# Optimization experiments

Hardware: AMD Instinct MI355X
Metric: run time of the kernel (lower is better)

Reference implementation:

```python
import jax, jax.numpy as jnp
import numpy as np

EPS = 1e-7

def segment_softmax(logits, seg, num_segments):
    # Numerically-stable softmax over edges grouped by destination node,
    # applied independently per feature column (logits: [E, D]).
    m = jax.ops.segment_max(logits, seg, num_segments=num_segments)  # [N, D]
    e = jnp.exp(logits - m[seg])                                     # [E, D]
    s = jax.ops.segment_sum(e, seg, num_segments=num_segments)       # [N, D]
    return e / s[seg]

def setup_inputs() -> dict:
    key = jax.random.key(0)
    N, E, D_IN, D_OUT = 50000, 800000, 64, 64
    ks = jax.random.split(key, 4)
    x = jax.random.normal(ks[0], (N, D_IN), dtype=jnp.float32)
    edge_index = jax.random.randint(ks[1], (2, E), 0, N, dtype=jnp.int64)
    # nn.Linear(in_feat, out_feat) params
    W = jax.random.normal(ks[2], (D_OUT, D_IN), dtype=jnp.float32) * (1.0 / np.sqrt(D_IN))
    b = jax.random.normal(ks[3], (D_OUT,), dtype=jnp.float32) * 0.01
    beta = jnp.ones((1,), dtype=jnp.float32)  # aggr='softmax_sg' beta parameter
    return {"x": x, "W": W, "b": b, "beta": beta, "edge_index": edge_index}

def reference(x, W, b, beta, edge_index):
    N = x.shape[0]
    dst = edge_index[0]  # scatter / softmax segment ids
    src = edge_index[1]  # gather ids
    # gather + ReLU + eps
    edge_msg = jax.nn.relu(x[src]) + EPS                    # [E, D]
    # softmax_sg aggregation: softmax of beta*msg over incoming edges of each dst
    a = segment_softmax(beta * edge_msg, dst, N)            # [E, D]
    h = jax.ops.segment_sum(edge_msg * a, dst, num_segments=N)  # [N, D]
    # final Linear
    return h @ W.T + b
```

## Files before the change

### kernel.cpp

```cpp
#include <hip/hip_runtime.h>
#include <hip/hip_fp16.h>

#define EPS 1e-7f
#define EPB 4096
#define CSTRIDE 16
#define SUBB 4
#define GS 65

__device__ __forceinline__ void pack_body(const float4* __restrict__ x4,
                                          short4* __restrict__ xh, int i, int nq) {
    if (i < nq) {
        float4 v = x4[i];
        short4 o;
        o.x = __half_as_short(__float2half_rn(fmaxf(v.x, 0.f) + EPS));
        o.y = __half_as_short(__float2half_rn(fmaxf(v.y, 0.f) + EPS));
        o.z = __half_as_short(__float2half_rn(fmaxf(v.z, 0.f) + EPS));
        o.w = __half_as_short(__float2half_rn(fmaxf(v.w, 0.f) + EPS));
        xh[i] = o;
    }
}

__global__ __launch_bounds__(256) void part_kernel(const float4* __restrict__ x4,
                                                   short4* __restrict__ xh, int nq,
                                                   int packBlocks,
                                                   const int* __restrict__ ei, int E,
                                                   int CAPB,
                                                   int* __restrict__ cursor,
                                                   unsigned int* __restrict__ partArr) {
    int bb = blockIdx.x;
    int tid = threadIdx.x;
    if (bb < packBlocks) {
        pack_body(x4, xh, bb * 256 + tid, nq);
        return;
    }
    __shared__ int hist[256];
    __shared__ int off[256];
    int blk = bb - packBlocks;
    hist[tid] = 0;
    __syncthreads();

    int base = blk * EPB;
    int dd[16], ss[16], bk[16], rk[16];
    #pragma unroll
    for (int k = 0; k < 16; ++k) {
        int e = base + k * 256 + tid;
        bk[k] = -1;
        if (e < E) {
            dd[k] = ei[e];
            ss[k] = ei[E + e];
            bk[k] = dd[k] >> 8;
            rk[k] = atomicAdd(&hist[bk[k]], 1);
        }
    }
    __syncthreads();
    int hv = hist[tid];
    if (hv > 0) off[tid] = atomicAdd(&cursor[tid * CSTRIDE], hv);
    __syncthreads();
    #pragma unroll
    for (int k = 0; k < 16; ++k) {
        if (bk[k] >= 0) {
            int idx = off[bk[k]] + rk[k];
            if (idx < CAPB)
                partArr[(size_t)bk[k] * CAPB + idx] =
                    ((unsigned int)dd[k] << 16) | (unsigned int)(ss[k] & 0xFFFF);
        }
    }
}

__global__ __launch_bounds__(256) void build_kernel(const unsigned int* __restrict__ partArr,
                                                    const int* __restrict__ cursor,
                                                    int CAPB,
                                                    unsigned short* __restrict__ slots,
                                                    int* __restrict__ deg) {
    __shared__ int c[256];
    __shared__ int base[256];
    int tid = threadIdx.x;
    int bkt = blockIdx.x >> 2;
    int sub = blockIdx.x & (SUBB - 1);
    c[tid] = 0;
    __syncthreads();

    int cnt = cursor[bkt * CSTRIDE];
    if (cnt > CAPB) cnt = CAPB;
    int lo = (cnt * sub) >> 2;
    int hi = (cnt * (sub + 1)) >> 2;
    const unsigned int* pa = partArr + (size_t)bkt * CAPB;

    for (int i = lo + tid; i < hi; i += 256)
        atomicAdd(&c[(pa[i] >> 16) & 255], 1);
    __syncthreads();
    int cc = c[tid];
    base[tid] = (cc > 0) ? atomicAdd(&deg[(bkt << 8) + tid], cc) : 0;
    c[tid] = 0;
    __syncthreads();
    for (int i = lo + tid; i < hi; i += 256) {
        unsigned int u = pa[i];
        int d = u >> 16;
        int r = base[d & 255] + atomicAdd(&c[d & 255], 1);
        if (r < 64) slots[((size_t)d << 6) + r] = (unsigned short)(u & 0xFFFF);
    }
}

__global__ __launch_bounds__(512) void main_kernel(const __half* __restrict__ xh,
                                                   const float* __restrict__ beta_p,
                                                   const int* __restrict__ deg,
                                                   const unsigned short* __restrict__ slots,
                                                   const float* __restrict__ W,
                                                   const float* __restrict__ bias,
                                                   float* __restrict__ out, int N) {
    __shared__ float hl[32 * GS];
    __shared__ float Wt[64 * GS];
    int tid  = threadIdx.x;
    int lane = tid & 63;
    int w    = tid >> 6;
    int n0   = blockIdx.x * 32;
    float beta = beta_p[0];

    #pragma unroll
    for (int kk = 0; kk < 2; ++kk) {
        int i4 = kk * 512 + tid;
        int rj = i4 >> 4;
        int d0 = (i4 & 15) * 4;
        float4 wv = *(const float4*)(W + (size_t)i4 * 4);
        Wt[(d0 + 0) * GS + rj] = wv.x;
        Wt[(d0 + 1) * GS + rj] = wv.y;
        Wt[(d0 + 2) * GS + rj] = wv.z;
        Wt[(d0 + 3) * GS + rj] = wv.w;
    }

    #pragma unroll
    for (int pp = 0; pp < 2; ++pp) {
        int la = (w << 2) + (pp << 1);
        int na = n0 + la, nb = na + 1;
        int nca = (na < N) ? na : (N - 1);
        int ncb = (nb < N) ? nb : (N - 1);
        unsigned short rawA = slots[((size_t)nca << 6) + lane];
        unsigned short rawB = slots[((size_t)ncb << 6) + lane];
        int dgA = deg[nca];
        int dgB = deg[ncb];
        if (dgA > 64) dgA = 64;
        if (dgB > 64) dgB = 64;
        int idA = (lane < dgA) ? (int)rawA : 0;
        int idB = (lane < dgB) ? (int)rawB : 0;
        int dgm = (dgA > dgB) ? dgA : dgB;

        float sA = 0.f, tA = 0.f, sB = 0.f, tB = 0.f;
        #define ACCV(wv, j, dgX, sX, tX) { float m = __half2float(wv);          \
            float e = __expf(beta * m); e = (i + (j) < dgX) ? e : 0.0f;         \
            sX += e; tX = fmaf(m, e, tX); }
        for (int i = 0; i < dgm; i += 8) {
            const __half* a0 = xh + (__builtin_amdgcn_readlane(idA, i + 0) << 6);
            const __half* a1 = xh + (__builtin_amdgcn_readlane(idA, i + 1) << 6);
            const __half* a2 = xh + (__builtin_amdgcn_readlane(idA, i + 2) << 6);
            const __half* a3 = xh + (__builtin_amdgcn_readlane(idA, i + 3) << 6);
            const __half* a4 = xh + (__builtin_amdgcn_readlane(idA, i + 4) << 6);
            const __half* a5 = xh + (__builtin_amdgcn_readlane(idA, i + 5) << 6);
            const __half* a6 = xh + (__builtin_amdgcn_readlane(idA, i + 6) << 6);
            const __half* a7 = xh + (__builtin_amdgcn_readlane(idA, i + 7) << 6);
            const __half* b0 = xh + (__builtin_amdgcn_readlane(idB, i + 0) << 6);
            const __half* b1 = xh + (__builtin_amdgcn_readlane(idB, i + 1) << 6);
            const __half* b2 = xh + (__builtin_amdgcn_readlane(idB, i + 2) << 6);
            const __half* b3 = xh + (__builtin_amdgcn_readlane(idB, i + 3) << 6);
            const __half* b4 = xh + (__builtin_amdgcn_readlane(idB, i + 4) << 6);
            const __half* b5 = xh + (__builtin_amdgcn_readlane(idB, i + 5) << 6);
            const __half* b6 = xh + (__builtin_amdgcn_readlane(idB, i + 6) << 6);
            const __half* b7 = xh + (__builtin_amdgcn_readlane(idB, i + 7) << 6);
            __half wa0 = a0[lane], wa1 = a1[lane], wa2 = a2[lane], wa3 = a3[lane];
            __half wa4 = a4[lane], wa5 = a5[lane], wa6 = a6[lane], wa7 = a7[lane];
            __half wb0 = b0[lane], wb1 = b1[lane], wb2 = b2[lane], wb3 = b3[lane];
            __half wb4 = b4[lane], wb5 = b5[lane], wb6 = b6[lane], wb7 = b7[lane];
            ACCV(wa0, 0, dgA, sA, tA) ACCV(wa1, 1, dgA, sA, tA)
            ACCV(wa2, 2, dgA, sA, tA) ACCV(wa3, 3, dgA, sA, tA)
            ACCV(wa4, 4, dgA, sA, tA) ACCV(wa5, 5, dgA, sA, tA)
            ACCV(wa6, 6, dgA, sA, tA) ACCV(wa7, 7, dgA, sA, tA)
            ACCV(wb0, 0, dgB, sB, tB) ACCV(wb1, 1, dgB, sB, tB)
            ACCV(wb2, 2, dgB, sB, tB) ACCV(wb3, 3, dgB, sB, tB)
            ACCV(wb4, 4, dgB, sB, tB) ACCV(wb5, 5, dgB, sB, tB)
            ACCV(wb6, 6, dgB, sB, tB) ACCV(wb7, 7, dgB, sB, tB)
        }
        #undef ACCV
        hl[la * GS + lane]       = (dgA > 0) ? (tA / sA) : 0.0f;
        hl[(la + 1) * GS + lane] = (dgB > 0) ? (tB / sB) : 0.0f;
    }
    __syncthreads();

    int c4 = tid & 15;
    int r  = tid >> 4;
    float4 bv = *(const float4*)(bias + c4 * 4);
    float a0 = bv.x, a1 = bv.y, a2 = bv.z, a3 = bv.w;
    #pragma unroll 8
    for (int d = 0; d < 64; ++d) {
        float h  = hl[r * GS + d];
        float w0 = Wt[d * GS + c4 * 4 + 0];
        float w1 = Wt[d * GS + c4 * 4 + 1];
        float w2 = Wt[d * GS + c4 * 4 + 2];
        float w3 = Wt[d * GS + c4 * 4 + 3];
        a0 = fmaf(h, w0, a0); a1 = fmaf(h, w1, a1);
        a2 = fmaf(h, w2, a2); a3 = fmaf(h, w3, a3);
    }
    int row = n0 + r;
    if (row < N)
        *(float4*)(out + (size_t)row * 64 + c4 * 4) = make_float4(a0, a1, a2, a3);
}

extern "C" void kernel_launch(void* const* d_in, const int* in_sizes, int n_in,
                              void* d_out, int out_size, void* d_ws, size_t ws_size,
                              hipStream_t stream) {
    const float* x      = (const float*)d_in[0];
    const float* W      = (const float*)d_in[1];
    const float* b      = (const float*)d_in[2];
    const float* beta_p = (const float*)d_in[3];
    const int*   ei     = (const int*)d_in[4];

    int NT = in_sizes[0];
    int N  = NT / 64;
    int E  = in_sizes[4] / 2;

    int NBK = (N + 255) >> 8;
    int NP  = NBK << 8;
    int pblocks = (NT / 4 + 255) / 256;
    int eblocks = (E + EPB - 1) / EPB;

    size_t curB   = (size_t)NBK * CSTRIDE * 4;
    size_t fixedB = curB + (size_t)NP * 4 + (size_t)NT * 2 + (size_t)NP * 64 * 2;
    int CAPB = (int)(((size_t)2 * E / NBK + 255) & ~(size_t)255);
    if (ws_size < fixedB + (size_t)NBK * CAPB * 4) {
        size_t avail = (ws_size > fixedB) ? (ws_size - fixedB) : 0;
        int fitc = (int)(avail / ((size_t)NBK * 4));
        CAPB = (fitc / 64) * 64;
        if (CAPB <= 0) return;
    }

    char* p = (char*)d_ws;
    int* cursor           = (int*)p;              p += curB;
    int* deg              = (int*)p;              p += (size_t)NP * 4;
    unsigned int* partArr = (unsigned int*)p;     p += (size_t)NBK * CAPB * 4;
    __half* xh            = (__half*)p;           p += (size_t)NT * 2;
    unsigned short* slots = (unsigned short*)p;

    hipMemsetAsync(cursor, 0, curB + (size_t)NP * 4, stream);

    part_kernel<<<pblocks + eblocks, 256, 0, stream>>>(
        (const float4*)x, (short4*)xh, NT / 4, pblocks, ei, E, CAPB, cursor, partArr);

    build_kernel<<<NBK * SUBB, 256, 0, stream>>>(partArr, cursor, CAPB, slots, deg);

    main_kernel<<<(N + 31) / 32, 512, 0, stream>>>(xh, beta_p, deg, slots, W, b,
                                                   (float*)d_out, N);
}
```

Measured before the change: 135.5 us.

## Software-pipeline neighbor gathers and hoist slot/degree loads in main kernel

```diff
diff --git a/kernel.cpp b/kernel.cpp
--- a/kernel.cpp
+++ b/kernel.cpp
@@ -100,6 +100,42 @@
         if (r < 64) slots[((size_t)d << 6) + r] = (unsigned short)(u & 0xFFFF);
     }
 }
+
+#define LOAD16(bA, bB, A0,A1,A2,A3,A4,A5,A6,A7, B0,B1,B2,B3,B4,B5,B6,B7)      \
+    { const __half* pa0 = xh + (__builtin_amdgcn_readlane(idA, (bA)+0) << 6); \
+      const __half* pa1 = xh + (__builtin_amdgcn_readlane(idA, (bA)+1) << 6); \
+      const __half* pa2 = xh + (__builtin_amdgcn_readlane(idA, (bA)+2) << 6); \
+      const __half* pa3 = xh + (__builtin_amdgcn_readlane(idA, (bA)+3) << 6); \
+      const __half* pa4 = xh + (__builtin_amdgcn_readlane(idA, (bA)+4) << 6); \
+      const __half* pa5 = xh + (__builtin_amdgcn_readlane(idA, (bA)+5) << 6); \
+      const __half* pa6 = xh + (__builtin_amdgcn_readlane(idA, (bA)+6) << 6); \
+      const __half* pa7 = xh + (__builtin_amdgcn_readlane(idA, (bA)+7) << 6); \
+      const __half* pb0 = xh + (__builtin_amdgcn_readlane(idB, (bB)+0) << 6); \
+      const __half* pb1 = xh + (__builtin_amdgcn_readlane(idB, (bB)+1) << 6); \
+      const __half* pb2 = xh + (__builtin_amdgcn_readlane(idB, (bB)+2) << 6); \
+      const __half* pb3 = xh + (__builtin_amdgcn_readlane(idB, (bB)+3) << 6); \
+      const __half* pb4 = xh + (__builtin_amdgcn_readlane(idB, (bB)+4) << 6); \
+      const __half* pb5 = xh + (__builtin_amdgcn_readlane(idB, (bB)+5) << 6); \
+      const __half* pb6 = xh + (__builtin_amdgcn_readlane(idB, (bB)+6) << 6); \
+      const __half* pb7 = xh + (__builtin_amdgcn_readlane(idB, (bB)+7) << 6); \
+      A0 = pa0[lane]; A1 = pa1[lane]; A2 = pa2[lane]; A3 = pa3[lane];         \
+      A4 = pa4[lane]; A5 = pa5[lane]; A6 = pa6[lane]; A7 = pa7[lane];         \
+      B0 = pb0[lane]; B1 = pb1[lane]; B2 = pb2[lane]; B3 = pb3[lane];         \
+      B4 = pb4[lane]; B5 = pb5[lane]; B6 = pb6[lane]; B7 = pb7[lane]; }
+
+#define ACC1(wv, idx, dgX, sX, tX) { float m = __half2float(wv);              \
+    float e = exp2f(bl2 * m); e = ((idx) < dgX) ? e : 0.0f;                   \
+    sX += e; tX = fmaf(m, e, tX); }
+
+#define ACC16(i0, A0,A1,A2,A3,A4,A5,A6,A7, B0,B1,B2,B3,B4,B5,B6,B7)          \
+    ACC1(A0,(i0)+0,dgA,sA,tA) ACC1(A1,(i0)+1,dgA,sA,tA)                      \
+    ACC1(A2,(i0)+2,dgA,sA,tA) ACC1(A3,(i0)+3,dgA,sA,tA)                      \
+    ACC1(A4,(i0)+4,dgA,sA,tA) ACC1(A5,(i0)+5,dgA,sA,tA)                      \
+    ACC1(A6,(i0)+6,dgA,sA,tA) ACC1(A7,(i0)+7,dgA,sA,tA)                      \
+    ACC1(B0,(i0)+0,dgB,sB,tB) ACC1(B1,(i0)+1,dgB,sB,tB)                      \
+    ACC1(B2,(i0)+2,dgB,sB,tB) ACC1(B3,(i0)+3,dgB,sB,tB)                      \
+    ACC1(B4,(i0)+4,dgB,sB,tB) ACC1(B5,(i0)+5,dgB,sB,tB)                      \
+    ACC1(B6,(i0)+6,dgB,sB,tB) ACC1(B7,(i0)+7,dgB,sB,tB)
 
 __global__ __launch_bounds__(512) void main_kernel(const __half* __restrict__ xh,
                                                    const float* __restrict__ beta_p,
@@ -114,7 +150,19 @@
     int lane = tid & 63;
     int w    = tid >> 6;
     int n0   = blockIdx.x * 32;
-    float beta = beta_p[0];
+    float bl2 = beta_p[0] * 1.44269504088896f;
+
+    int la0 = w << 2;
+    int q0 = n0 + la0, q1 = q0 + 1, q2 = q0 + 2, q3 = q0 + 3;
+    int c0 = (q0 < N) ? q0 : (N - 1);
+    int c1 = (q1 < N) ? q1 : (N - 1);
+    int c2 = (q2 < N) ? q2 : (N - 1);
+    int c3 = (q3 < N) ? q3 : (N - 1);
+    unsigned short rw0 = slots[((size_t)c0 << 6) + lane];
+    unsigned short rw1 = slots[((size_t)c1 << 6) + lane];
+    unsigned short rw2 = slots[((size_t)c2 << 6) + lane];
+    unsigned short rw3 = slots[((size_t)c3 << 6) + lane];
+    int dq0 = deg[c0], dq1 = deg[c1], dq2 = deg[c2], dq3 = deg[c3];
 
     #pragma unroll
     for (int kk = 0; kk < 2; ++kk) {
@@ -128,57 +176,48 @@
         Wt[(d0 + 3) * GS + rj] = wv.w;
     }
 
+    if (dq0 > 64) dq0 = 64;
+    if (dq1 > 64) dq1 = 64;
+    if (dq2 > 64) dq2 = 64;
+    if (dq3 > 64) dq3 = 64;
+    int id0 = (lane < dq0) ? (int)rw0 : 0;
+    int id1 = (lane < dq1) ? (int)rw1 : 0;
+    int id2 = (lane < dq2) ? (int)rw2 : 0;
+    int id3 = (lane < dq3) ? (int)rw3 : 0;
+
     #pragma unroll
     for (int pp = 0; pp < 2; ++pp) {
-        int la = (w << 2) + (pp << 1);
-        int na = n0 + la, nb = na + 1;
-        int nca = (na < N) ? na : (N - 1);
-        int ncb = (nb < N) ? nb : (N - 1);
-        unsigned short rawA = slots[((size_t)nca << 6) + lane];
-        unsigned short rawB = slots[((size_t)ncb << 6) + lane];
-        int dgA = deg[nca];
-        int dgB = deg[ncb];
-        if (dgA > 64) dgA = 64;
-        if (dgB > 64) dgB = 64;
-        int idA = (lane < dgA) ? (int)rawA : 0;
-        int idB = (lane < dgB) ? (int)rawB : 0;
+        const int idA = pp ? id2 : id0;
+        const int idB = pp ? id3 : id1;
+        const int dgA = pp ? dq2 : dq0;
+        const int dgB = pp ? dq3 : dq1;
+        const int la  = la0 + (pp << 1);
+        float sA = 0.f, tA = 0.f, sB = 0.f, tB = 0.f;
         int dgm = (dgA > dgB) ? dgA : dgB;
 
-        float sA = 0.f, tA = 0.f, sB = 0.f, tB = 0.f;
-        #define ACCV(wv, j, dgX, sX, tX) { float m = __half2float(wv);          \
-            float e = __expf(beta * m); e = (i + (j) < dgX) ? e : 0.0f;         \
-            sX += e; tX = fmaf(m, e, tX); }
-        for (int i = 0; i < dgm; i += 8) {
-            const __half* a0 = xh + (__builtin_amdgcn_readlane(idA, i + 0) << 6);
-            const __half* a1 = xh + (__builtin_amdgcn_readlane(idA, i + 1) << 6);
-            const __half* a2 = xh + (__builtin_amdgcn_readlane(idA, i + 2) << 6);
-            const __half* a3 = xh + (__builtin_amdgcn_readlane(idA, i + 3) << 6);
-            const __half* a4 = xh + (__builtin_amdgcn_readlane(idA, i + 4) << 6);
-            const __half* a5 = xh + (__builtin_amdgcn_readlane(idA, i + 5) << 6);
-            const __half* a6 = xh + (__builtin_amdgcn_readlane(idA, i + 6) << 6);
-            const __half* a7 = xh + (__builtin_amdgcn_readlane(idA, i + 7) << 6);
-            const __half* b0 = xh + (__builtin_amdgcn_readlane(idB, i + 0) << 6);
-            const __half* b1 = xh + (__builtin_amdgcn_readlane(idB, i + 1) << 6);
-            const __half* b2 = xh + (__builtin_amdgcn_readlane(idB, i + 2) << 6);
-            const __half* b3 = xh + (__builtin_amdgcn_readlane(idB, i + 3) << 6);
-            const __half* b4 = xh + (__builtin_amdgcn_readlane(idB, i + 4) << 6);
-            const __half* b5 = xh + (__builtin_amdgcn_readlane(idB, i + 5) << 6);
-            const __half* b6 = xh + (__builtin_amdgcn_readlane(idB, i + 6) << 6);
-            const __half* b7 = xh + (__builtin_amdgcn_readlane(idB, i + 7) << 6);
-            __half wa0 = a0[lane], wa1 = a1[lane], wa2 = a2[lane], wa3 = a3[lane];
-            __half wa4 = a4[lane], wa5 = a5[lane], wa6 = a6[lane], wa7 = a7[lane];
-            __half wb0 = b0[lane], wb1 = b1[lane], wb2 = b2[lane], wb3 = b3[lane];
-            __half wb4 = b4[lane], wb5 = b5[lane], wb6 = b6[lane], wb7 = b7[lane];
-            ACCV(wa0, 0, dgA, sA, tA) ACCV(wa1, 1, dgA, sA, tA)
-            ACCV(wa2, 2, dgA, sA, tA) ACCV(wa3, 3, dgA, sA, tA)
-            ACCV(wa4, 4, dgA, sA, tA) ACCV(wa5, 5, dgA, sA, tA)
-            ACCV(wa6, 6, dgA, sA, tA) ACCV(wa7, 7, dgA, sA, tA)
-            ACCV(wb0, 0, dgB, sB, tB) ACCV(wb1, 1, dgB, sB, tB)
-            ACCV(wb2, 2, dgB, sB, tB) ACCV(wb3, 3, dgB, sB, tB)
-            ACCV(wb4, 4, dgB, sB, tB) ACCV(wb5, 5, dgB, sB, tB)
-            ACCV(wb6, 6, dgB, sB, tB) ACCV(wb7, 7, dgB, sB, tB)
+        __half cA0,cA1,cA2,cA3,cA4,cA5,cA6,cA7, cB0,cB1,cB2,cB3,cB4,cB5,cB6,cB7;
+        __half nA0,nA1,nA2,nA3,nA4,nA5,nA6,nA7, nB0,nB1,nB2,nB3,nB4,nB5,nB6,nB7;
+        if (dgm > 0) {
+            LOAD16(0, 0, cA0,cA1,cA2,cA3,cA4,cA5,cA6,cA7,
+                         cB0,cB1,cB2,cB3,cB4,cB5,cB6,cB7)
+            int i = 0;
+            while (true) {
+                int ip = (i + 8 < dgm) ? (i + 8) : 0;
+                LOAD16(ip, ip, nA0,nA1,nA2,nA3,nA4,nA5,nA6,nA7,
+                               nB0,nB1,nB2,nB3,nB4,nB5,nB6,nB7)
+                ACC16(i, cA0,cA1,cA2,cA3,cA4,cA5,cA6,cA7,
+                         cB0,cB1,cB2,cB3,cB4,cB5,cB6,cB7)
+                i += 8;
+                if (i >= dgm) break;
+                ip = (i + 8 < dgm) ? (i + 8) : 0;
+                LOAD16(ip, ip, cA0,cA1,cA2,cA3,cA4,cA5,cA6,cA7,
+                               cB0,cB1,cB2,cB3,cB4,cB5,cB6,cB7)
+                ACC16(i, nA0,nA1,nA2,nA3,nA4,nA5,nA6,nA7,
+                         nB0,nB1,nB2,nB3,nB4,nB5,nB6,nB7)
+                i += 8;
+                if (i >= dgm) break;
+            }
         }
-        #undef ACCV
         hl[la * GS + lane]       = (dgA > 0) ? (tA / sA) : 0.0f;
         hl[(la + 1) * GS + lane] = (dgB > 0) ? (tB / sB) : 0.0f;
     }
```

Result: slower. 152.8 us (+12.8%).
